# Kernel tuning notes

Measured on AMD Instinct MI355X. Metric: run time of the kernel, lower is better.

## Reference

```python
import jax, jax.numpy as jnp
import numpy as np

SIM = 100      # topk k
GCH = SIM + 1  # group size after concat
LCH = 80       # low-rank mid channels
D = 96         # embed dim


def setup_inputs() -> dict:
    key = jax.random.key(0)
    ks = jax.random.split(key, 14)
    b, N, W, p = 1, 4, 16, 128
    def lin(kw, kb, out_f, in_f):
        s = 1.0 / np.sqrt(in_f)
        w = jax.random.uniform(kw, (out_f, in_f), minval=-s, maxval=s, dtype=jnp.float32)
        bb = jax.random.uniform(kb, (out_f,), minval=-s, maxval=s, dtype=jnp.float32)
        return w, bb
    attn = jax.random.normal(ks[0], (b, N, W, 1, p, p), dtype=jnp.float32)
    v = jax.random.normal(ks[1], (b, N, W, 1, p, D), dtype=jnp.float32)
    mb = jax.random.normal(ks[2], (LCH, 1), dtype=jnp.float32)
    w_sub, b_sub = lin(ks[3], ks[4], LCH, GCH)
    w_up, b_up = lin(ks[5], ks[6], GCH, LCH)
    w_q, b_q = lin(ks[7], ks[8], D, D)
    w_k, b_k = lin(ks[9], ks[10], D, D)
    w_o, b_o = lin(ks[11], ks[12], D, D)
    return {"attn": attn, "v": v, "mb": mb, "w_sub": w_sub, "b_sub": b_sub,
            "w_up": w_up, "b_up": b_up, "w_q": w_q, "b_q": b_q,
            "w_k": w_k, "b_k": b_k, "w_o": w_o, "b_o": b_o}


def reference(attn, v, mb, w_sub, b_sub, w_up, b_up, w_q, b_q, w_k, b_k, w_o, b_o):
    b, N, W, _, p, _ = attn.shape
    c = v.shape[-1]
    # topk + scatter(binary mask) + boolean-compact gather == gather v rows at
    # ascending-sorted topk indices (boolean masking preserves index order).
    _, idx = jax.lax.top_k(attn, SIM)            # [b,N,W,1,p,SIM]
    idx = jnp.sort(idx[:, :, :, 0], axis=-1)     # [b,N,W,p,SIM]
    vq = v[:, :, :, 0]                            # [b,N,W,p,c]
    bI = jnp.arange(b)[:, None, None, None, None]
    nI = jnp.arange(N)[None, :, None, None, None]
    wI = jnp.arange(W)[None, None, :, None, None]
    gathered = vq[bI, nI, wI, idx]                # [b,N,W,p,SIM,c]
    group3d = jnp.concatenate([vq[:, :, :, :, None, :], gathered], axis=4)  # [b,N,W,p,GCH,c]
    # ChannelAttention (memory_blocks=1): pool over c, low-rank memory bank
    y = jnp.mean(group3d, axis=-1)                # [b,N,W,p,GCH]
    lr = y @ w_sub.T + b_sub                      # [b,N,W,p,LCH]
    f1 = (lr @ mb) * (LCH ** -0.5)                # [b,N,W,p,1]
    f_dic = jax.nn.softmax(f1[..., None, :], axis=-1)   # [b,N,W,p,1,1] == 1
    y1 = f_dic * mb[:, 0]                         # [b,N,W,p,1,LCH]
    scale = jax.nn.sigmoid(y1 @ w_up.T + b_up)    # [b,N,W,p,1,GCH]
    scale = scale.reshape(b, N, W, p, GCH, 1)     # matches torch .view(b,N,Nwin,p,n,-1)
    g = group3d * scale
    # StructuralSelfAttention (num_heads=1): query = group element 0, keys/values = rest
    x = g[:, :, :, :, :1, :]                      # [b,N,W,p,1,c]
    yk = g[:, :, :, :, 1:, :]                     # [b,N,W,p,SIM,c]
    q = x @ w_q.T + b_q
    k = yk @ w_k.T + b_k
    scores = jnp.einsum('bnwpqc,bnwpkc->bnwpqk', q, k) / jnp.sqrt(jnp.float32(c))
    wgt = jax.nn.softmax(scores, axis=-1)
    out = jnp.einsum('bnwpqk,bnwpkc->bnwpqc', wgt, yk)  # v = y (no v_proj in source)
    out = out.reshape(b, N, W, p, c)
    return out @ w_o.T + b_o
```

## Files before the change

### kernel.cpp

```cpp
#include <hip/hip_runtime.h>
#include <hip/hip_bf16.h>

#define NW 64
#define P 128
#define D 96
#define GCH 101
#define SIM 100
#define LCH 80
#define RSQRT96 0.10206207261596577f

#define WS_SCALE 0
#define WS_Q     128
#define WS_KT    (128 + 786432)
#define WS_VO    (128 + 2*786432)

__global__ __launch_bounds__(256) void proj_kernel(const float* __restrict__ v,
    const float* __restrict__ wq, const float* __restrict__ bq,
    const float* __restrict__ wk, const float* __restrict__ wo,
    const float* __restrict__ mb, const float* __restrict__ w_up,
    const float* __restrict__ b_up, float* __restrict__ ws) {
  int bid = blockIdx.x;
  int nw = bid / 6;
  int rem = bid - nw * 6;
  int pj = rem >> 1;
  int half = rem & 1;
  const float* W = (pj == 0) ? wq : (pj == 1) ? wk : wo;
  __shared__ float sWt[96 * 100];
  __shared__ float sV[64 * 100];
  int tid = threadIdx.x;
  for (int idx = tid; idx < 96 * 96; idx += 256) {
    int c = idx / 96, d = idx - c * 96;
    sWt[d * 100 + c] = W[idx];
  }
  float scale0 = 0.0f;
  if (pj == 0) {
    float acc = b_up[0];
    for (int j = 0; j < LCH; ++j) acc += w_up[j] * mb[j];
    scale0 = 1.0f / (1.0f + __expf(-acc));
  }
  const float* vq = v + nw * (P * D) + half * (64 * D);
  for (int idx = tid; idx < 64 * 96; idx += 256) {
    int r = idx / 96, d = idx - r * 96;
    sV[r * 100 + d] = vq[idx];
  }
  __syncthreads();
  int ty = tid >> 3;
  int tx = tid & 7;
  float acc0[12], acc1[12];
#pragma unroll
  for (int j = 0; j < 12; ++j) { acc0[j] = 0.f; acc1[j] = 0.f; }
  for (int d = 0; d < 96; ++d) {
    float v0 = sV[(ty * 2 + 0) * 100 + d];
    float v1 = sV[(ty * 2 + 1) * 100 + d];
    const float4* wp = (const float4*)&sWt[d * 100 + tx * 12];
    float4 w0 = wp[0], w1 = wp[1], w2 = wp[2];
    float wbuf[12] = {w0.x,w0.y,w0.z,w0.w, w1.x,w1.y,w1.z,w1.w, w2.x,w2.y,w2.z,w2.w};
#pragma unroll
    for (int j = 0; j < 12; ++j) {
      acc0[j] += v0 * wbuf[j];
      acc1[j] += v1 * wbuf[j];
    }
  }
  float* outQ  = ws + WS_Q  + nw * (P * D);
  float* outKt = ws + WS_KT + nw * (P * D);
  float* outO  = ws + WS_VO + nw * (P * D);
  int r0 = half * 64 + ty * 2;
#pragma unroll
  for (int a = 0; a < 2; ++a) {
    int r = r0 + a;
    const float* accp = a ? acc1 : acc0;
#pragma unroll
    for (int j = 0; j < 12; ++j) {
      int c = tx * 12 + j;
      float val = accp[j];
      if (pj == 0)      outQ[r * 96 + c] = scale0 * val + bq[c];
      else if (pj == 1) outKt[c * P + r] = val;
      else              outO[r * 96 + c] = val;
    }
  }
  if (bid == 0 && tid < GCH) {
    float acc = b_up[tid];
    for (int j = 0; j < LCH; ++j) acc += w_up[tid * LCH + j] * mb[j];
    ws[WS_SCALE + tid] = 1.0f / (1.0f + __expf(-acc));
  }
}

__global__ __launch_bounds__(128) void attn_kernel(const float* __restrict__ attn,
    const float* __restrict__ bo, const float* __restrict__ ws,
    float* __restrict__ out) {
  int bid = blockIdx.x;
  int nw = bid >> 5;
  int pt = bid & 31;
  int p0 = pt * 4;
  int tid = threadIdx.x;
  int wave = tid >> 6, lane = tid & 63;
  __shared__ float sQ[4 * 96];
  __shared__ unsigned long long sKey[4 * 128];
  __shared__ float sT[4 * 128];
  __shared__ float sScale[104];
  __shared__ unsigned long long sB[4];
  __shared__ float sMx[4][2];
  __shared__ float sSm[4][2];
  const float* Qg = ws + WS_Q  + nw * (P * D);
  const float* Kt = ws + WS_KT + nw * (P * D);
  const float* VO = ws + WS_VO + nw * (P * D);
  if (tid < GCH) sScale[tid] = ws[WS_SCALE + tid];
  for (int idx = tid; idx < 4 * 96; idx += 128) sQ[idx] = Qg[p0 * 96 + idx];
  unsigned long long mykey[4];
#pragma unroll
  for (int r = 0; r < 4; ++r) {
    float a = attn[((size_t)(nw * 128 + p0 + r)) * 128 + tid];
    unsigned u = __float_as_uint(a);
    unsigned msk = (u & 0x80000000u) ? 0xFFFFFFFFu : 0x80000000u;
    unsigned long long k =
        (((unsigned long long)(u ^ msk)) << 32) | (unsigned)(127 - tid);
    mykey[r] = k;
    sKey[r * 128 + tid] = k;
  }
  __syncthreads();
  float acc[4] = {0.f, 0.f, 0.f, 0.f};
  for (int c = 0; c < 96; ++c) {
    float kv = Kt[c * P + tid];
#pragma unroll
    for (int r = 0; r < 4; ++r) acc[r] += sQ[r * 96 + c] * kv;
  }
  int cnt[4] = {0, 0, 0, 0};
#pragma unroll 4
  for (int j = 0; j < 128; ++j) {
#pragma unroll
    for (int r = 0; r < 4; ++r)
      cnt[r] += (sKey[r * 128 + j] > mykey[r]) ? 1 : 0;
  }
  bool keep[4];
  unsigned long long bal[4];
#pragma unroll
  for (int r = 0; r < 4; ++r) {
    keep[r] = cnt[r] < SIM;
    bal[r] = __ballot(keep[r]);
  }
  if (wave == 0 && lane == 0) {
#pragma unroll
    for (int r = 0; r < 4; ++r) sB[r] = bal[r];
  }
  __syncthreads();
  float sval[4], sc[4], mx[4];
#pragma unroll
  for (int r = 0; r < 4; ++r) {
    int pos = __popcll(bal[r] & ((1ull << lane) - 1ull)) +
              (wave ? __popcll(sB[r]) : 0);
    sval[r] = keep[r] ? sScale[1 + pos] : 0.f;
    sc[r] = keep[r] ? sval[r] * acc[r] * RSQRT96 : -1e30f;
    mx[r] = sc[r];
#pragma unroll
    for (int off = 32; off > 0; off >>= 1) mx[r] = fmaxf(mx[r], __shfl_xor(mx[r], off));
    if (lane == 0) sMx[r][wave] = mx[r];
  }
  __syncthreads();
  float e[4], sm[4];
#pragma unroll
  for (int r = 0; r < 4; ++r) {
    float M = fmaxf(sMx[r][0], sMx[r][1]);
    e[r] = keep[r] ? __expf(sc[r] - M) : 0.f;
    sm[r] = e[r];
#pragma unroll
    for (int off = 32; off > 0; off >>= 1) sm[r] += __shfl_xor(sm[r], off);
    if (lane == 0) sSm[r][wave] = sm[r];
  }
  __syncthreads();
#pragma unroll
  for (int r = 0; r < 4; ++r) {
    float S = sSm[r][0] + sSm[r][1];
    sT[r * 128 + tid] = keep[r] ? (e[r] / S) * sval[r] : 0.f;
  }
  __syncthreads();
  if (tid < D) {
    float facc[4] = {0.f, 0.f, 0.f, 0.f};
    for (int j = 0; j < 128; ++j) {
      float vo = VO[j * D + tid];
#pragma unroll
      for (int r = 0; r < 4; ++r) facc[r] += sT[r * 128 + j] * vo;
    }
    float bb = bo[tid];
#pragma unroll
    for (int r = 0; r < 4; ++r)
      out[((size_t)(nw * 128 + p0 + r)) * D + tid] = facc[r] + bb;
  }
}

extern "C" void kernel_launch(void* const* d_in, const int* in_sizes, int n_in,
                              void* d_out, int out_size, void* d_ws, size_t ws_size,
                              hipStream_t stream) {
  const float* attn = (const float*)d_in[0];
  const float* v    = (const float*)d_in[1];
  const float* mb   = (const float*)d_in[2];
  const float* w_up = (const float*)d_in[5];
  const float* b_up = (const float*)d_in[6];
  const float* w_q  = (const float*)d_in[7];
  const float* b_q  = (const float*)d_in[8];
  const float* w_k  = (const float*)d_in[9];
  const float* w_o  = (const float*)d_in[11];
  const float* b_o  = (const float*)d_in[12];
  float* out = (float*)d_out;
  float* ws = (float*)d_ws;

  hipLaunchKernelGGL(proj_kernel, dim3(NW * 6), dim3(256), 0, stream,
                     v, w_q, b_q, w_k, w_o, mb, w_up, b_up, ws);
  hipLaunchKernelGGL(attn_kernel, dim3(NW * 32), dim3(128), 0, stream,
                     attn, b_o, ws, out);
}
```

Measured before the change: 56.20 us.

## Rewrite projection with register-held weights and attention as wave-per-row-group

The projection kernel now keeps one weight row per thread in 96 registers and streams V rows from global memory. It drops the shared-memory tiles and uses a small shared transpose only for K. The attention kernel gives each wave four query rows and handles both 64-key halves in registers. Top-k ranks are computed by reloading attn values rather than from shared memory, and the softmax uses whole-wave shuffles and readlane broadcasts with no block syncs. This removes barriers and shared traffic, at the cost of high register pressure, repeated global/L1 loads and redundant FMA lanes in the output loop.

```diff
diff --git a/kernel.cpp b/kernel.cpp
--- a/kernel.cpp
+++ b/kernel.cpp
@@ -4,6 +4,7 @@
 #define NW 64
 #define P 128
 #define D 96
+#define PD (P*D)
 #define GCH 101
 #define SIM 100
 #define LCH 80
@@ -14,7 +15,15 @@
 #define WS_KT    (128 + 786432)
 #define WS_VO    (128 + 2*786432)
 
-__global__ __launch_bounds__(256) void proj_kernel(const float* __restrict__ v,
+typedef unsigned long long ull;
+
+__device__ __forceinline__ ull make_key(float a, int idx) {
+  unsigned u = __float_as_uint(a);
+  unsigned msk = (u & 0x80000000u) ? 0xFFFFFFFFu : 0x80000000u;
+  return (((ull)(u ^ msk)) << 32) | (unsigned)(127 - idx);
+}
+
+__global__ __launch_bounds__(128) void proj_kernel(const float* __restrict__ v,
     const float* __restrict__ wq, const float* __restrict__ bq,
     const float* __restrict__ wk, const float* __restrict__ wo,
     const float* __restrict__ mb, const float* __restrict__ w_up,
@@ -22,168 +31,160 @@
   int bid = blockIdx.x;
   int nw = bid / 6;
   int rem = bid - nw * 6;
-  int pj = rem >> 1;
-  int half = rem & 1;
+  int pj = rem >> 1, half = rem & 1;
+  int t = threadIdx.x;
   const float* W = (pj == 0) ? wq : (pj == 1) ? wk : wo;
-  __shared__ float sWt[96 * 100];
-  __shared__ float sV[64 * 100];
-  int tid = threadIdx.x;
-  for (int idx = tid; idx < 96 * 96; idx += 256) {
-    int c = idx / 96, d = idx - c * 96;
-    sWt[d * 100 + c] = W[idx];
-  }
-  float scale0 = 0.0f;
+  float wreg[96];
+  {
+    const float4* wp = (const float4*)(W + (t < 96 ? t : 0) * 96);
+#pragma unroll
+    for (int i = 0; i < 24; ++i) {
+      float4 x = wp[i];
+      wreg[4*i+0] = x.x; wreg[4*i+1] = x.y; wreg[4*i+2] = x.z; wreg[4*i+3] = x.w;
+    }
+  }
+  float scale0 = 0.f, bias = 0.f;
   if (pj == 0) {
-    float acc = b_up[0];
-    for (int j = 0; j < LCH; ++j) acc += w_up[j] * mb[j];
-    scale0 = 1.0f / (1.0f + __expf(-acc));
-  }
-  const float* vq = v + nw * (P * D) + half * (64 * D);
-  for (int idx = tid; idx < 64 * 96; idx += 256) {
-    int r = idx / 96, d = idx - r * 96;
-    sV[r * 100 + d] = vq[idx];
-  }
-  __syncthreads();
-  int ty = tid >> 3;
-  int tx = tid & 7;
-  float acc0[12], acc1[12];
-#pragma unroll
-  for (int j = 0; j < 12; ++j) { acc0[j] = 0.f; acc1[j] = 0.f; }
-  for (int d = 0; d < 96; ++d) {
-    float v0 = sV[(ty * 2 + 0) * 100 + d];
-    float v1 = sV[(ty * 2 + 1) * 100 + d];
-    const float4* wp = (const float4*)&sWt[d * 100 + tx * 12];
-    float4 w0 = wp[0], w1 = wp[1], w2 = wp[2];
-    float wbuf[12] = {w0.x,w0.y,w0.z,w0.w, w1.x,w1.y,w1.z,w1.w, w2.x,w2.y,w2.z,w2.w};
-#pragma unroll
-    for (int j = 0; j < 12; ++j) {
-      acc0[j] += v0 * wbuf[j];
-      acc1[j] += v1 * wbuf[j];
-    }
-  }
-  float* outQ  = ws + WS_Q  + nw * (P * D);
-  float* outKt = ws + WS_KT + nw * (P * D);
-  float* outO  = ws + WS_VO + nw * (P * D);
-  int r0 = half * 64 + ty * 2;
-#pragma unroll
-  for (int a = 0; a < 2; ++a) {
-    int r = r0 + a;
-    const float* accp = a ? acc1 : acc0;
-#pragma unroll
-    for (int j = 0; j < 12; ++j) {
-      int c = tx * 12 + j;
-      float val = accp[j];
-      if (pj == 0)      outQ[r * 96 + c] = scale0 * val + bq[c];
-      else if (pj == 1) outKt[c * P + r] = val;
-      else              outO[r * 96 + c] = val;
-    }
-  }
-  if (bid == 0 && tid < GCH) {
-    float acc = b_up[tid];
-    for (int j = 0; j < LCH; ++j) acc += w_up[tid * LCH + j] * mb[j];
-    ws[WS_SCALE + tid] = 1.0f / (1.0f + __expf(-acc));
-  }
-}
-
-__global__ __launch_bounds__(128) void attn_kernel(const float* __restrict__ attn,
+    float a = b_up[0];
+    for (int j = 0; j < LCH; ++j) a += w_up[j] * mb[j];
+    scale0 = 1.f / (1.f + __expf(-a));
+    bias = (t < 96) ? bq[t] : 0.f;
+  }
+  __shared__ float sK[96 * 65];
+  const float* Vb = v + (size_t)(nw * P + half * 64) * D;
+  float* outp = ws + ((pj == 0) ? WS_Q : (pj == 1) ? WS_KT : WS_VO) + nw * PD;
+  for (int r = 0; r < 64; ++r) {
+    const float* Vr = Vb + r * D;
+    float a0 = 0.f, a1 = 0.f, a2 = 0.f, a3 = 0.f;
+#pragma unroll
+    for (int i = 0; i < 24; ++i) {
+      a0 += Vr[4*i+0] * wreg[4*i+0];
+      a1 += Vr[4*i+1] * wreg[4*i+1];
+      a2 += Vr[4*i+2] * wreg[4*i+2];
+      a3 += Vr[4*i+3] * wreg[4*i+3];
+    }
+    float acc = (a0 + a1) + (a2 + a3);
+    if (t < 96) {
+      if (pj == 0)      outp[(half*64 + r) * D + t] = scale0 * acc + bias;
+      else if (pj == 2) outp[(half*64 + r) * D + t] = acc;
+      else              sK[t * 65 + r] = acc;
+    }
+  }
+  if (pj == 1) {
+    __syncthreads();
+    for (int idx = t; idx < 96 * 64; idx += 128) {
+      int c = idx >> 6, r = idx & 63;
+      outp[c * P + half * 64 + r] = sK[c * 65 + r];
+    }
+  }
+  if (bid == 0 && t < GCH) {
+    float a = b_up[t];
+    for (int j = 0; j < LCH; ++j) a += w_up[t * LCH + j] * mb[j];
+    ws[WS_SCALE + t] = 1.f / (1.f + __expf(-a));
+  }
+}
+
+__global__ __launch_bounds__(256) void attn_kernel(const float* __restrict__ attn,
     const float* __restrict__ bo, const float* __restrict__ ws,
     float* __restrict__ out) {
-  int bid = blockIdx.x;
-  int nw = bid >> 5;
-  int pt = bid & 31;
-  int p0 = pt * 4;
   int tid = threadIdx.x;
-  int wave = tid >> 6, lane = tid & 63;
-  __shared__ float sQ[4 * 96];
-  __shared__ unsigned long long sKey[4 * 128];
-  __shared__ float sT[4 * 128];
-  __shared__ float sScale[104];
-  __shared__ unsigned long long sB[4];
-  __shared__ float sMx[4][2];
-  __shared__ float sSm[4][2];
-  const float* Qg = ws + WS_Q  + nw * (P * D);
-  const float* Kt = ws + WS_KT + nw * (P * D);
-  const float* VO = ws + WS_VO + nw * (P * D);
-  if (tid < GCH) sScale[tid] = ws[WS_SCALE + tid];
-  for (int idx = tid; idx < 4 * 96; idx += 128) sQ[idx] = Qg[p0 * 96 + idx];
-  unsigned long long mykey[4];
+  int wv = tid >> 6, lane = tid & 63;
+  int nw = blockIdx.x >> 3;
+  int rt = blockIdx.x & 7;
+  int p0 = rt * 16 + wv * 4;
+  const float* Kt  = ws + WS_KT + nw * PD;
+  const float* VO  = ws + WS_VO + nw * PD;
+  const float* Qb  = ws + WS_Q  + nw * PD + p0 * D;
+  const float* Ab  = attn + (size_t)(nw * P + p0) * P;
+  const float* scl = ws + WS_SCALE;
+
+  ull k0[4], k1[4];
 #pragma unroll
   for (int r = 0; r < 4; ++r) {
-    float a = attn[((size_t)(nw * 128 + p0 + r)) * 128 + tid];
-    unsigned u = __float_as_uint(a);
-    unsigned msk = (u & 0x80000000u) ? 0xFFFFFFFFu : 0x80000000u;
-    unsigned long long k =
-        (((unsigned long long)(u ^ msk)) << 32) | (unsigned)(127 - tid);
-    mykey[r] = k;
-    sKey[r * 128 + tid] = k;
-  }
-  __syncthreads();
-  float acc[4] = {0.f, 0.f, 0.f, 0.f};
-  for (int c = 0; c < 96; ++c) {
-    float kv = Kt[c * P + tid];
-#pragma unroll
-    for (int r = 0; r < 4; ++r) acc[r] += sQ[r * 96 + c] * kv;
-  }
-  int cnt[4] = {0, 0, 0, 0};
+    k0[r] = make_key(Ab[r * P + lane], lane);
+    k1[r] = make_key(Ab[r * P + 64 + lane], 64 + lane);
+  }
+
+  float s0[4] = {0,0,0,0}, s1[4] = {0,0,0,0};
+#pragma unroll 8
+  for (int c = 0; c < D; ++c) {
+    float kv0 = Kt[c * P + lane];
+    float kv1 = Kt[c * P + 64 + lane];
+#pragma unroll
+    for (int r = 0; r < 4; ++r) {
+      float q = Qb[r * D + c];
+      s0[r] += q * kv0;
+      s1[r] += q * kv1;
+    }
+  }
+
+  int c0[4] = {0,0,0,0}, c1[4] = {0,0,0,0};
 #pragma unroll 4
-  for (int j = 0; j < 128; ++j) {
-#pragma unroll
-    for (int r = 0; r < 4; ++r)
-      cnt[r] += (sKey[r * 128 + j] > mykey[r]) ? 1 : 0;
-  }
-  bool keep[4];
-  unsigned long long bal[4];
+  for (int j = 0; j < P; ++j) {
+#pragma unroll
+    for (int r = 0; r < 4; ++r) {
+      ull kj = make_key(Ab[r * P + j], j);
+      c0[r] += (kj > k0[r]) ? 1 : 0;
+      c1[r] += (kj > k1[r]) ? 1 : 0;
+    }
+  }
+
+  float t0[4], t1[4];
+  ull lm = (1ull << lane) - 1ull;
 #pragma unroll
   for (int r = 0; r < 4; ++r) {
-    keep[r] = cnt[r] < SIM;
-    bal[r] = __ballot(keep[r]);
-  }
-  if (wave == 0 && lane == 0) {
-#pragma unroll
-    for (int r = 0; r < 4; ++r) sB[r] = bal[r];
-  }
-  __syncthreads();
-  float sval[4], sc[4], mx[4];
+    bool kp0 = c0[r] < SIM, kp1 = c1[r] < SIM;
+    ull b0 = __ballot(kp0), b1 = __ballot(kp1);
+    int pos0 = __popcll(b0 & lm);
+    int pos1 = __popcll(b0) + __popcll(b1 & lm);
+    float sv0 = kp0 ? scl[1 + pos0] : 0.f;
+    float sv1 = kp1 ? scl[1 + pos1] : 0.f;
+    float x0 = kp0 ? sv0 * s0[r] * RSQRT96 : -1e30f;
+    float x1 = kp1 ? sv1 * s1[r] * RSQRT96 : -1e30f;
+    float m = fmaxf(x0, x1);
+#pragma unroll
+    for (int off = 1; off < 64; off <<= 1) m = fmaxf(m, __shfl_xor(m, off));
+    float e0 = kp0 ? __expf(x0 - m) : 0.f;
+    float e1 = kp1 ? __expf(x1 - m) : 0.f;
+    float s = e0 + e1;
+#pragma unroll
+    for (int off = 1; off < 64; off <<= 1) s += __shfl_xor(s, off);
+    float inv = 1.f / s;
+    t0[r] = e0 * inv * sv0;
+    t1[r] = e1 * inv * sv1;
+  }
+
+  float o0[4] = {0,0,0,0}, o1[4] = {0,0,0,0};
+  int lane2 = (lane < 32) ? (64 + lane) : 95;
+#pragma unroll 4
+  for (int j = 0; j < 64; ++j) {
+    float vo0 = VO[j * D + lane];
+    float vo1 = VO[j * D + lane2];
+#pragma unroll
+    for (int r = 0; r < 4; ++r) {
+      float tv = __int_as_float(__builtin_amdgcn_readlane(__float_as_int(t0[r]), j));
+      o0[r] += tv * vo0;
+      o1[r] += tv * vo1;
+    }
+  }
+#pragma unroll 4
+  for (int j = 0; j < 64; ++j) {
+    float vo0 = VO[(64 + j) * D + lane];
+    float vo1 = VO[(64 + j) * D + lane2];
+#pragma unroll
+    for (int r = 0; r < 4; ++r) {
+      float tv = __int_as_float(__builtin_amdgcn_readlane(__float_as_int(t1[r]), j));
+      o0[r] += tv * vo0;
+      o1[r] += tv * vo1;
+    }
+  }
+  float bb0 = bo[lane];
+  float bb1 = bo[lane2];
+  float* op = out + (size_t)(nw * P + p0) * D;
 #pragma unroll
   for (int r = 0; r < 4; ++r) {
-    int pos = __popcll(bal[r] & ((1ull << lane) - 1ull)) +
-              (wave ? __popcll(sB[r]) : 0);
-    sval[r] = keep[r] ? sScale[1 + pos] : 0.f;
-    sc[r] = keep[r] ? sval[r] * acc[r] * RSQRT96 : -1e30f;
-    mx[r] = sc[r];
-#pragma unroll
-    for (int off = 32; off > 0; off >>= 1) mx[r] = fmaxf(mx[r], __shfl_xor(mx[r], off));
-    if (lane == 0) sMx[r][wave] = mx[r];
-  }
-  __syncthreads();
-  float e[4], sm[4];
-#pragma unroll
-  for (int r = 0; r < 4; ++r) {
-    float M = fmaxf(sMx[r][0], sMx[r][1]);
-    e[r] = keep[r] ? __expf(sc[r] - M) : 0.f;
-    sm[r] = e[r];
-#pragma unroll
-    for (int off = 32; off > 0; off >>= 1) sm[r] += __shfl_xor(sm[r], off);
-    if (lane == 0) sSm[r][wave] = sm[r];
-  }
-  __syncthreads();
-#pragma unroll
-  for (int r = 0; r < 4; ++r) {
-    float S = sSm[r][0] + sSm[r][1];
-    sT[r * 128 + tid] = keep[r] ? (e[r] / S) * sval[r] : 0.f;
-  }
-  __syncthreads();
-  if (tid < D) {
-    float facc[4] = {0.f, 0.f, 0.f, 0.f};
-    for (int j = 0; j < 128; ++j) {
-      float vo = VO[j * D + tid];
-#pragma unroll
-      for (int r = 0; r < 4; ++r) facc[r] += sT[r * 128 + j] * vo;
-    }
-    float bb = bo[tid];
-#pragma unroll
-    for (int r = 0; r < 4; ++r)
-      out[((size_t)(nw * 128 + p0 + r)) * D + tid] = facc[r] + bb;
+    op[r * D + lane] = o0[r] + bb0;
+    if (lane < 32) op[r * D + 64 + lane] = o1[r] + bb1;
   }
 }
 
@@ -203,8 +204,8 @@
   float* out = (float*)d_out;
   float* ws = (float*)d_ws;
 
-  hipLaunchKernelGGL(proj_kernel, dim3(NW * 6), dim3(256), 0, stream,
+  hipLaunchKernelGGL(proj_kernel, dim3(NW * 6), dim3(128), 0, stream,
                      v, w_q, b_q, w_k, w_o, mb, w_up, b_up, ws);
-  hipLaunchKernelGGL(attn_kernel, dim3(NW * 32), dim3(128), 0, stream,
+  hipLaunchKernelGGL(attn_kernel, dim3(NW * 8), dim3(256), 0, stream,
                      attn, b_o, ws, out);
 }
```

Result: slower. 137.7 us (+145.1%).
